# Kernel optimization log

Hardware: AMD Instinct MI355X
Metric: run time of the kernel (lower is better)

Reference implementation:

```python
import jax, jax.numpy as jnp
import numpy as np

NEG_BIG = -1e10
LEAKY_ALPHA = 0.2

def setup_inputs() -> dict:
    key = jax.random.key(0)
    k1, k2, k3, k4 = jax.random.split(key, 4)
    B, N, F, H = 8, 2048, 128, 4
    X = jax.random.normal(k1, (B, N, F), dtype=jnp.float32)
    A = jax.random.bernoulli(k2, 0.06, (B, N, N)).astype(jnp.float32)
    A = jnp.maximum(A, jnp.eye(N, dtype=jnp.float32)[None])
    attn_self = jax.random.normal(k3, (H, F), dtype=jnp.float32) * 0.1
    attn_neigh = jax.random.normal(k4, (H, F), dtype=jnp.float32) * 0.1
    return {"X": X, "A": A, "attn_self": attn_self, "attn_neigh": attn_neigh}

def reference(X, A, attn_self, attn_neigh):
    # mode 0, concat reduction, tanh activation (applied per head, as in call_mode0)
    B, N, F = X.shape
    H = attn_self.shape[0]
    a_self = jnp.einsum('bnf,hf->bhn', X, attn_self)   # [B,H,N]
    a_neigh = jnp.einsum('bnf,hf->bhn', X, attn_neigh)  # [B,H,N]
    dense = a_self[:, :, :, None] + a_neigh[:, :, None, :]  # [B,H,N,N]
    dense = jnp.where(dense >= 0, dense, LEAKY_ALPHA * dense)  # leaky relu 0.2
    mask = jnp.where(A == 0.0, NEG_BIG, 0.0)[:, None, :, :]   # [B,1,N,N]
    attn = jax.nn.softmax(dense + mask, axis=-1)               # [B,H,N,N]
    feats = jnp.einsum('bhnm,bmf->bhnf', attn, X)              # [B,H,N,F]
    feats = jnp.tanh(feats)
    # concat heads on feature axis -> [B,N,H*F]
    return feats.transpose(0, 2, 1, 3).reshape(B, N, H * F)
```

## Files before the change

kernel.cpp:

```cpp
#include <hip/hip_runtime.h>
#include <hip/hip_bf16.h>
#include <math.h>

#define N_NODES 2048
#define F_DIM   128
#define H_HEADS 4
#define B_BATCH 8
#define LEAKY   0.2f

__device__ __forceinline__ float tanh_fast(float x) {
    const float e = __expf(2.0f * x);
    return 1.0f - 2.0f / (e + 1.0f);
}

__global__ __launch_bounds__(256) void gat_proj(const float* __restrict__ X,
                                                const float* __restrict__ wS,
                                                const float* __restrict__ wN,
                                                float* __restrict__ aSt,
                                                float* __restrict__ aNt) {
    const int wave = threadIdx.x >> 6;
    const int lane = threadIdx.x & 63;
    const int row  = blockIdx.x * 4 + wave;
    const float* xr = X + (size_t)row * F_DIM;
    const float x0 = xr[lane];
    const float x1 = xr[lane + 64];
    float4 ps4, pn4;
    float* psv = (float*)&ps4;
    float* pnv = (float*)&pn4;
#pragma unroll
    for (int h = 0; h < H_HEADS; ++h) {
        float ps = x0 * wS[h * F_DIM + lane] + x1 * wS[h * F_DIM + 64 + lane];
        float pn = x0 * wN[h * F_DIM + lane] + x1 * wN[h * F_DIM + 64 + lane];
#pragma unroll
        for (int off = 32; off > 0; off >>= 1) {
            ps += __shfl_xor(ps, off);
            pn += __shfl_xor(pn, off);
        }
        psv[h] = ps;
        pnv[h] = pn;
    }
    if (lane == 0) {
        ((float4*)aSt)[row] = ps4;
        ((float4*)aNt)[row] = pn4;
    }
}

__global__ __launch_bounds__(256) void gat_gmax(const float* __restrict__ aNt,
                                                float* __restrict__ gmax) {
    const int b = blockIdx.x;
    const int tid = threadIdx.x;
    const int lane = tid & 63;
    const int wv = tid >> 6;
    __shared__ float4 s_part[4];
    float4 m = make_float4(-1e30f, -1e30f, -1e30f, -1e30f);
    const float4* src = (const float4*)aNt + (size_t)b * N_NODES;
    for (int n = tid; n < N_NODES; n += 256) {
        const float4 v = src[n];
        m.x = fmaxf(m.x, v.x); m.y = fmaxf(m.y, v.y);
        m.z = fmaxf(m.z, v.z); m.w = fmaxf(m.w, v.w);
    }
#pragma unroll
    for (int off = 32; off > 0; off >>= 1) {
        m.x = fmaxf(m.x, __shfl_xor(m.x, off));
        m.y = fmaxf(m.y, __shfl_xor(m.y, off));
        m.z = fmaxf(m.z, __shfl_xor(m.z, off));
        m.w = fmaxf(m.w, __shfl_xor(m.w, off));
    }
    if (lane == 0) s_part[wv] = m;
    __syncthreads();
    if (tid == 0) {
        float4 r = s_part[0];
#pragma unroll
        for (int w = 1; w < 4; ++w) {
            r.x = fmaxf(r.x, s_part[w].x); r.y = fmaxf(r.y, s_part[w].y);
            r.z = fmaxf(r.z, s_part[w].z); r.w = fmaxf(r.w, s_part[w].w);
        }
        ((float4*)gmax)[b] = r;
    }
}

__global__ __launch_bounds__(256, 8) void gat_main(const float* __restrict__ X,
                                                   const float* __restrict__ A,
                                                   const float* __restrict__ aSt,
                                                   const float* __restrict__ aNt,
                                                   const float* __restrict__ gmax,
                                                   float* __restrict__ out) {
    const int tid = threadIdx.x;
    const int row = blockIdx.x;
    const int b = row >> 11;
    const int lane = tid & 63;
    const int wv = tid >> 6;

    __shared__ short s_idx[N_NODES];
    __shared__ float s_p[256 * 4];
    __shared__ float s_red[4 * 512];
    __shared__ int   s_wtot[4];
    __shared__ float s_M[4];
    __shared__ float s_sv[4];
    __shared__ float s_scr[16];

    const float4* Arow = (const float4*)(A + (size_t)row * N_NODES);
    const float4 a0 = Arow[tid * 2];
    const float4 a1 = Arow[tid * 2 + 1];

    if (tid < 4) {
        const float sv = aSt[(size_t)row * 4 + tid];
        const float g = gmax[b * 4 + tid];
        float v = sv + g;
        v = fmaxf(v, LEAKY * v);
        s_M[tid] = v;
        s_sv[tid] = sv;
    }

    const float av[8] = {a0.x, a0.y, a0.z, a0.w, a1.x, a1.y, a1.z, a1.w};
    int c = 0;
#pragma unroll
    for (int k = 0; k < 8; ++k) c += (av[k] != 0.0f) ? 1 : 0;

    int incl = c;
#pragma unroll
    for (int d = 1; d < 64; d <<= 1) {
        const int u = __shfl_up(incl, d);
        if (lane >= d) incl += u;
    }
    if (lane == 63) s_wtot[wv] = incl;
    __syncthreads();
    int wbase = 0;
#pragma unroll
    for (int w = 0; w < 4; ++w) wbase += (w < wv) ? s_wtot[w] : 0;
    const int cnt = s_wtot[0] + s_wtot[1] + s_wtot[2] + s_wtot[3];
    int pos = wbase + (incl - c);
#pragma unroll
    for (int k = 0; k < 8; ++k) {
        if (av[k] != 0.0f) s_idx[pos++] = (short)(tid * 8 + k);
    }
    __syncthreads();

    float acc[4][4];
#pragma unroll
    for (int h = 0; h < 4; ++h)
#pragma unroll
        for (int fi = 0; fi < 4; ++fi) acc[h][fi] = 0.0f;
    float lsum[4] = {0.0f, 0.0f, 0.0f, 0.0f};

    const int jsub = tid >> 5;
    const int f4 = tid & 31;
    const float* Xb = X + (size_t)b * N_NODES * F_DIM;
    const float4* aNb4 = (const float4*)aNt + (size_t)b * N_NODES;

    for (int base = 0; base < cnt; base += 256) {
        const int clen = min(256, cnt - base);
        if (tid < clen) {
            const int m = s_idx[base + tid];
            const float4 t = aNb4[m];
            const float tv[4] = {t.x, t.y, t.z, t.w};
            float4 p4;
            float* pp = (float*)&p4;
#pragma unroll
            for (int h = 0; h < H_HEADS; ++h) {
                float v = s_sv[h] + tv[h];
                v = fmaxf(v, LEAKY * v);
                const float p = __expf(v - s_M[h]);
                pp[h] = p;
                lsum[h] += p;
            }
            ((float4*)s_p)[tid] = p4;
        }
        __syncthreads();
#pragma unroll 4
        for (int j = jsub; j < clen; j += 8) {
            const float4 pv = ((const float4*)s_p)[j];
            const int m = s_idx[base + j];
            const float4 xv = *(const float4*)&Xb[(size_t)m * F_DIM + f4 * 4];
            const float pr[4] = {pv.x, pv.y, pv.z, pv.w};
            const float xr[4] = {xv.x, xv.y, xv.z, xv.w};
#pragma unroll
            for (int h = 0; h < 4; ++h)
#pragma unroll
                for (int fi = 0; fi < 4; ++fi)
                    acc[h][fi] = fmaf(pr[h], xr[fi], acc[h][fi]);
        }
        __syncthreads();
    }

#pragma unroll
    for (int h = 0; h < H_HEADS; ++h) {
        float v = lsum[h];
#pragma unroll
        for (int off = 32; off > 0; off >>= 1) v += __shfl_xor(v, off);
        if (lane == 0) s_scr[wv * 4 + h] = v;
    }
#pragma unroll
    for (int h = 0; h < 4; ++h)
#pragma unroll
        for (int fi = 0; fi < 4; ++fi)
            acc[h][fi] += __shfl_xor(acc[h][fi], 32);
    if (lane < 32) {
        float4* red4 = (float4*)s_red;
#pragma unroll
        for (int h = 0; h < 4; ++h)
            red4[wv * 128 + h * 32 + f4] =
                make_float4(acc[h][0], acc[h][1], acc[h][2], acc[h][3]);
    }
    __syncthreads();

    const int hf = tid * 2;
    const int h = tid >> 6;
    const float l = s_scr[h] + s_scr[4 + h] + s_scr[8 + h] + s_scr[12 + h];
    const float invl = 1.0f / l;
    float v0 = 0.0f, v1 = 0.0f;
#pragma unroll
    for (int w = 0; w < 4; ++w) {
        v0 += s_red[w * 512 + hf];
        v1 += s_red[w * 512 + hf + 1];
    }
    float2 o;
    o.x = tanh_fast(v0 * invl);
    o.y = tanh_fast(v1 * invl);
    *(float2*)&out[(size_t)row * 512 + hf] = o;
}

extern "C" void kernel_launch(void* const* d_in, const int* in_sizes, int n_in,
                              void* d_out, int out_size, void* d_ws, size_t ws_size,
                              hipStream_t stream) {
    const float* X  = (const float*)d_in[0];
    const float* A  = (const float*)d_in[1];
    const float* wS = (const float*)d_in[2];
    const float* wN = (const float*)d_in[3];
    float* out = (float*)d_out;

    float* aSt = (float*)d_ws;
    float* aNt = aSt + (size_t)B_BATCH * N_NODES * H_HEADS;
    float* gmx = aNt + (size_t)B_BATCH * N_NODES * H_HEADS;

    gat_proj<<<(B_BATCH * N_NODES) / 4, 256, 0, stream>>>(X, wS, wN, aSt, aNt);
    gat_gmax<<<B_BATCH, 256, 0, stream>>>(aNt, gmx);
    gat_main<<<B_BATCH * N_NODES, 256, 0, stream>>>(X, A, aSt, aNt, gmx, out);
}
```

Baseline: 105.5 us.

## Software-pipeline neighbor X gathers with padded chunks and precomputed byte offsets

Restructures the aggregation loop in gat_main into a software pipeline. X rows are loaded two iterations ahead, and the first row load is issued before the softmax-weight barrier. Byte offsets are stored in shared memory and the chunk is zero-padded to a multiple of 8, which removes bounds checks and index conversion from the inner loop. The aim is to hide gather latency, at the cost of more registers and an extra X load per padded slot.

```diff
diff --git a/kernel.cpp b/kernel.cpp
--- a/kernel.cpp
+++ b/kernel.cpp
@@ -79,6 +79,26 @@
     }
 }
 
+#define FMA16(PV, XV)                                        \
+    do {                                                     \
+        acc[0][0] = fmaf((PV).x, (XV).x, acc[0][0]);         \
+        acc[0][1] = fmaf((PV).x, (XV).y, acc[0][1]);         \
+        acc[0][2] = fmaf((PV).x, (XV).z, acc[0][2]);         \
+        acc[0][3] = fmaf((PV).x, (XV).w, acc[0][3]);         \
+        acc[1][0] = fmaf((PV).y, (XV).x, acc[1][0]);         \
+        acc[1][1] = fmaf((PV).y, (XV).y, acc[1][1]);         \
+        acc[1][2] = fmaf((PV).y, (XV).z, acc[1][2]);         \
+        acc[1][3] = fmaf((PV).y, (XV).w, acc[1][3]);         \
+        acc[2][0] = fmaf((PV).z, (XV).x, acc[2][0]);         \
+        acc[2][1] = fmaf((PV).z, (XV).y, acc[2][1]);         \
+        acc[2][2] = fmaf((PV).z, (XV).z, acc[2][2]);         \
+        acc[2][3] = fmaf((PV).z, (XV).w, acc[2][3]);         \
+        acc[3][0] = fmaf((PV).w, (XV).x, acc[3][0]);         \
+        acc[3][1] = fmaf((PV).w, (XV).y, acc[3][1]);         \
+        acc[3][2] = fmaf((PV).w, (XV).z, acc[3][2]);         \
+        acc[3][3] = fmaf((PV).w, (XV).w, acc[3][3]);         \
+    } while (0)
+
 __global__ __launch_bounds__(256, 8) void gat_main(const float* __restrict__ X,
                                                    const float* __restrict__ A,
                                                    const float* __restrict__ aSt,
@@ -91,13 +111,14 @@
     const int lane = tid & 63;
     const int wv = tid >> 6;
 
-    __shared__ short s_idx[N_NODES];
-    __shared__ float s_p[256 * 4];
-    __shared__ float s_red[4 * 512];
-    __shared__ int   s_wtot[4];
-    __shared__ float s_M[4];
-    __shared__ float s_sv[4];
-    __shared__ float s_scr[16];
+    __shared__ short  s_idx[N_NODES];
+    __shared__ float4 s_p4[272];
+    __shared__ int    s_off[272];
+    __shared__ float  s_red[4 * 512];
+    __shared__ int    s_wtot[4];
+    __shared__ float  s_M[4];
+    __shared__ float  s_sv[4];
+    __shared__ float  s_scr[16];
 
     const float4* Arow = (const float4*)(A + (size_t)row * N_NODES);
     const float4 a0 = Arow[tid * 2];
@@ -145,41 +166,66 @@
 
     const int jsub = tid >> 5;
     const int f4 = tid & 31;
-    const float* Xb = X + (size_t)b * N_NODES * F_DIM;
+    const char* XbB = (const char*)(X + (size_t)b * N_NODES * F_DIM) + (f4 << 4);
     const float4* aNb4 = (const float4*)aNt + (size_t)b * N_NODES;
 
     for (int base = 0; base < cnt; base += 256) {
         const int clen = min(256, cnt - base);
-        if (tid < clen) {
-            const int m = s_idx[base + tid];
-            const float4 t = aNb4[m];
-            const float tv[4] = {t.x, t.y, t.z, t.w};
+        const int plen = (clen + 7) & ~7;
+
+        const int pj = (jsub < clen) ? (int)s_idx[base + jsub] : 0;
+        const float4 xv_pre = *(const float4*)(XbB + ((unsigned)pj << 9));
+
+        if (tid < plen) {
             float4 p4;
-            float* pp = (float*)&p4;
-#pragma unroll
-            for (int h = 0; h < H_HEADS; ++h) {
-                float v = s_sv[h] + tv[h];
-                v = fmaxf(v, LEAKY * v);
-                const float p = __expf(v - s_M[h]);
-                pp[h] = p;
-                lsum[h] += p;
+            int offv;
+            if (tid < clen) {
+                const int m = s_idx[base + tid];
+                const float4 t = aNb4[m];
+                const float tv[4] = {t.x, t.y, t.z, t.w};
+                float* pp = (float*)&p4;
+#pragma unroll
+                for (int h = 0; h < H_HEADS; ++h) {
+                    float v = s_sv[h] + tv[h];
+                    v = fmaxf(v, LEAKY * v);
+                    const float p = __expf(v - s_M[h]);
+                    pp[h] = p;
+                    lsum[h] += p;
+                }
+                offv = m << 9;
+            } else {
+                p4 = make_float4(0.0f, 0.0f, 0.0f, 0.0f);
+                offv = 0;
             }
-            ((float4*)s_p)[tid] = p4;
+            s_p4[tid] = p4;
+            s_off[tid] = offv;
+        }
+        if (tid < 16) {
+            s_p4[plen + tid] = make_float4(0.0f, 0.0f, 0.0f, 0.0f);
+            s_off[plen + tid] = 0;
         }
         __syncthreads();
-#pragma unroll 4
-        for (int j = jsub; j < clen; j += 8) {
-            const float4 pv = ((const float4*)s_p)[j];
-            const int m = s_idx[base + j];
-            const float4 xv = *(const float4*)&Xb[(size_t)m * F_DIM + f4 * 4];
-            const float pr[4] = {pv.x, pv.y, pv.z, pv.w};
-            const float xr[4] = {xv.x, xv.y, xv.z, xv.w};
-#pragma unroll
-            for (int h = 0; h < 4; ++h)
-#pragma unroll
-                for (int fi = 0; fi < 4; ++fi)
-                    acc[h][fi] = fmaf(pr[h], xr[fi], acc[h][fi]);
-        }
+
+        const int nit = plen >> 3;
+        float4 pv  = s_p4[jsub];
+        float4 pvn = s_p4[jsub + 8];
+        const int off1 = s_off[jsub + 8];
+        int offA = s_off[jsub + 16];
+        float4 xv  = xv_pre;
+        float4 xvn = *(const float4*)(XbB + (unsigned)off1);
+
+        for (int i = 0; i + 2 < nit; ++i) {
+            const int jb = jsub + ((i + 2) << 3);
+            const float4 xvnn = *(const float4*)(XbB + (unsigned)offA);
+            const float4 pvnn = s_p4[jb];
+            const int offB = s_off[jb + 8];
+            FMA16(pv, xv);
+            pv = pvn; pvn = pvnn;
+            xv = xvn; xvn = xvnn;
+            offA = offB;
+        }
+        FMA16(pv, xv);
+        FMA16(pvn, xvn);
         __syncthreads();
     }
 
```

Result: slower. 118.7 us (+12.5%).
